# Kernel optimization log

Hardware: AMD Instinct MI355X
Metric: run time of the kernel (lower is better)

## Reference

```python
import jax, jax.numpy as jnp
import numpy as np

DIM = 768
DEPTH = 12
HEADS = 12
PATCH = 16
IMG = 256
CIN = 3
HID = 4 * DIM
EPS = 1e-6


def rmsnorm(x, w):
    return x * jax.lax.rsqrt(jnp.mean(x * x, axis=-1, keepdims=True) + EPS) * w


def ste(x, xq):
    # straight-through estimator: forward uses quantized value
    return x + jax.lax.stop_gradient(xq - x)


def bit_linear(x, w):
    # BitNet b1.58: ternary weights (per-tensor absmean scale) + int8 per-token activations
    w_scale = jnp.mean(jnp.abs(w)) + 1e-5
    w_q = jnp.clip(jnp.round(w / w_scale), -1.0, 1.0) * w_scale
    w_dq = ste(w, w_q)
    x_scale = 127.0 / jnp.clip(jnp.max(jnp.abs(x), axis=-1, keepdims=True), 1e-5)
    x_q = jnp.clip(jnp.round(x * x_scale), -128.0, 127.0) / x_scale
    x_dq = ste(x, x_q)
    return x_dq @ w_dq.T


def time_embedding(t, t_w1, t_b1, t_w2, t_b2):
    half = DIM // 2
    freqs = jnp.exp(-jnp.log(10000.0) * jnp.arange(half, dtype=jnp.float32) / (half - 1))
    args = t[:, None] * freqs[None, :]
    emb = jnp.concatenate([jnp.sin(args), jnp.cos(args)], axis=-1)
    h = jax.nn.gelu(emb @ t_w1.T + t_b1)
    return h @ t_w2.T + t_b2


def dit_block(x, t_emb, n1, qkv_w, proj_w, n2, fc1_w, fc2_w, ada_w, ada_b):
    B, N, C = x.shape
    hd = C // HEADS
    mod = jax.nn.silu(t_emb) @ ada_w.T + ada_b  # [B, 4*C]
    shift1, scale1, shift2, scale2 = jnp.split(mod, 4, axis=-1)
    # attention branch
    h = rmsnorm(x, n1)
    h = h * (1.0 + scale1[:, None, :]) + shift1[:, None, :]
    qkv = bit_linear(h, qkv_w).reshape(B, N, 3, HEADS, hd)
    q, k, v = qkv[:, :, 0], qkv[:, :, 1], qkv[:, :, 2]  # [B, N, H, hd]
    attn = jnp.einsum('bnhd,bmhd->bhnm', q, k) * (hd ** -0.5)
    attn = jax.nn.softmax(attn, axis=-1)
    o = jnp.einsum('bhnm,bmhd->bnhd', attn, v).reshape(B, N, C)
    x = x + bit_linear(o, proj_w)
    # mlp branch
    h = rmsnorm(x, n2)
    h = h * (1.0 + scale2[:, None, :]) + shift2[:, None, :]
    h = jax.nn.gelu(bit_linear(h, fc1_w))
    x = x + bit_linear(h, fc2_w)
    return x


def setup_inputs() -> dict:
    key = jax.random.key(0)
    ks = jax.random.split(key, 20)
    s = 0.02
    patch_dim = CIN * PATCH * PATCH
    inp = {
        'x': jax.random.normal(ks[0], (16, CIN, IMG, IMG), jnp.float32),
        't': jax.random.uniform(ks[1], (16,), jnp.float32) * 1000.0,
        'patch_w': jax.random.normal(ks[2], (DIM, patch_dim), jnp.float32) * s,
        'patch_b': jnp.zeros((DIM,), jnp.float32),
        'pos_embed': jax.random.normal(ks[3], (1, (IMG // PATCH) ** 2, DIM), jnp.float32) * s,
        't_w1': jax.random.normal(ks[4], (DIM, DIM), jnp.float32) * s,
        't_b1': jnp.zeros((DIM,), jnp.float32),
        't_w2': jax.random.normal(ks[5], (DIM, DIM), jnp.float32) * s,
        't_b2': jnp.zeros((DIM,), jnp.float32),
        'blk_norm1': jnp.ones((DEPTH, DIM), jnp.float32),
        'blk_qkv': jax.random.normal(ks[6], (DEPTH, 3 * DIM, DIM), jnp.float32) * s,
        'blk_proj': jax.random.normal(ks[7], (DEPTH, DIM, DIM), jnp.float32) * s,
        'blk_norm2': jnp.ones((DEPTH, DIM), jnp.float32),
        'blk_fc1': jax.random.normal(ks[8], (DEPTH, HID, DIM), jnp.float32) * s,
        'blk_fc2': jax.random.normal(ks[9], (DEPTH, DIM, HID), jnp.float32) * s,
        'blk_ada_w': jax.random.normal(ks[10], (DEPTH, 4 * DIM, DIM), jnp.float32) * s,
        'blk_ada_b': jnp.zeros((DEPTH, 4 * DIM), jnp.float32),
        'norm_w': jnp.ones((DIM,), jnp.float32),
        'head_w': jax.random.normal(ks[11], (patch_dim, DIM), jnp.float32) * s,
        'head_b': jnp.zeros((patch_dim,), jnp.float32),
    }
    return inp


def reference(x, t, patch_w, patch_b, pos_embed, t_w1, t_b1, t_w2, t_b2,
              blk_norm1, blk_qkv, blk_proj, blk_norm2, blk_fc1, blk_fc2,
              blk_ada_w, blk_ada_b, norm_w, head_w, head_b):
    B, C, H, W = x.shape
    p = PATCH
    h = H // p
    w = W // p
    # patchify: [B, C, H, W] -> [B, N, C*p*p]
    xp = x.reshape(B, C, h, p, w, p).transpose(0, 2, 4, 1, 3, 5).reshape(B, h * w, C * p * p)
    z = xp @ patch_w.T + patch_b + pos_embed
    t_emb = time_embedding(t, t_w1, t_b1, t_w2, t_b2)
    for i in range(DEPTH):
        z = dit_block(z, t_emb, blk_norm1[i], blk_qkv[i], blk_proj[i],
                      blk_norm2[i], blk_fc1[i], blk_fc2[i], blk_ada_w[i], blk_ada_b[i])
    z = rmsnorm(z, norm_w)
    z = z @ head_w.T + head_b  # [B, N, C*p*p]
    # unpatchify
    out = z.reshape(B, h, w, C, p, p).transpose(0, 3, 1, 4, 2, 5).reshape(B, C, H, W)
    return out
```

## Files before the change

kernel.cpp:

```cpp
#include <hip/hip_runtime.h>
#include <cstdint>

#define NTOK   4096
#define CDIM   768
#define NHID   3072
#define NHEADS 12

typedef int i32x4 __attribute__((ext_vector_type(4)));

__device__ __forceinline__ float4 ld4(const float* p){ return *(const float4*)(p); }

__device__ __forceinline__ float gelu_f(float x){
  float x3 = x*x*x;
  return 0.5f*x*(1.0f + tanhf(0.7978845608028654f*(x + 0.044715f*x3)));
}

template<bool ISMAX>
__device__ __forceinline__ float block_reduce(float v, float* red){
  #pragma unroll
  for (int o = 32; o > 0; o >>= 1){
    float w = __shfl_down(v, o);
    v = ISMAX ? fmaxf(v, w) : (v + w);
  }
  int wid = threadIdx.x >> 6;
  if ((threadIdx.x & 63) == 0) red[wid] = v;
  __syncthreads();
  float r = ISMAX ? fmaxf(fmaxf(red[0], red[1]), fmaxf(red[2], red[3]))
                  : (red[0] + red[1] + red[2] + red[3]);
  __syncthreads();
  return r;
}

__device__ __forceinline__ const float* layer_base(int type, int blk,
    const float* wqkv, const float* wproj, const float* wfc1, const float* wfc2,
    long* n_out, long* qoff_out)
{
  switch (type){
    case 0:  *n_out = 2304L*768; *qoff_out = 0;       return wqkv  + (long)blk*2304*768;
    case 1:  *n_out = 768L*768;  *qoff_out = 1769472; return wproj + (long)blk*768*768;
    case 2:  *n_out = 3072L*768; *qoff_out = 2359296; return wfc1  + (long)blk*3072*768;
    default: *n_out = 768L*3072; *qoff_out = 4718592; return wfc2  + (long)blk*768*3072;
  }
}

__global__ __launch_bounds__(256) void k_wabs_reduce(
  const float* __restrict__ wqkv, const float* __restrict__ wproj,
  const float* __restrict__ wfc1, const float* __restrict__ wfc2,
  float* __restrict__ acc)
{
  __shared__ float red[4];
  int layer = blockIdx.y, blk = layer >> 2, type = layer & 3;
  long n, qoff;
  const float* base = layer_base(type, blk, wqkv, wproj, wfc1, wfc2, &n, &qoff);
  long i0 = ((long)blockIdx.x*256 + threadIdx.x)*8;
  float s = 0.f;
  if (i0 < n){
    float4 a = ld4(base+i0), b = ld4(base+i0+4);
    s = fabsf(a.x)+fabsf(a.y)+fabsf(a.z)+fabsf(a.w)
      + fabsf(b.x)+fabsf(b.y)+fabsf(b.z)+fabsf(b.w);
  }
  s = block_reduce<false>(s, red);
  if (threadIdx.x == 0 && s != 0.f) atomicAdd(&acc[layer], s);
}

__global__ void k_wscale(const float* __restrict__ acc, float* __restrict__ wsc){
  int l = threadIdx.x;
  if (l < 48){
    const float cnt[4] = {2304.f*768.f, 768.f*768.f, 3072.f*768.f, 768.f*3072.f};
    wsc[l] = acc[l]/cnt[l & 3] + 1e-5f;
  }
}

__global__ __launch_bounds__(256) void k_wquant_write(
  const float* __restrict__ wqkv, const float* __restrict__ wproj,
  const float* __restrict__ wfc1, const float* __restrict__ wfc2,
  const float* __restrict__ wsc, signed char* __restrict__ wq)
{
  int layer = blockIdx.y, blk = layer >> 2, type = layer & 3;
  long n, qoff;
  const float* base = layer_base(type, blk, wqkv, wproj, wfc1, wfc2, &n, &qoff);
  long i0 = ((long)blockIdx.x*256 + threadIdx.x)*8;
  if (i0 >= n) return;
  signed char* dst = wq + (long)blk*7077888 + qoff;
  float ws = wsc[layer];
  float4 a = ld4(base+i0), b = ld4(base+i0+4);
  float v[8] = {a.x,a.y,a.z,a.w,b.x,b.y,b.z,b.w};
  long pk;
  char* pc = (char*)&pk;
  #pragma unroll
  for (int e = 0; e < 8; e++){
    float r = rintf(v[e] / ws);
    r = fminf(1.f, fmaxf(-1.f, r));
    pc[e] = (char)(int)r;
  }
  *(long*)(dst + i0) = pk;
}

__global__ __launch_bounds__(256) void k_patchify(const float* __restrict__ x, float* __restrict__ xp){
  int idx = blockIdx.x*256 + threadIdx.x;
  int col = idx % 768, row = idx / 768;
  int bb = row >> 8, pr = row & 255, ph = pr >> 4, pw = pr & 15;
  int c = col >> 8, rem = col & 255, ii = rem >> 4, jj = rem & 15;
  xp[idx] = x[(((long)(bb*3 + c) << 8) + (ph<<4) + ii)*256 + (pw<<4) + jj];
}

__global__ __launch_bounds__(256) void k_unpatchify(const float* __restrict__ H, float* __restrict__ out){
  int idx = blockIdx.x*256 + threadIdx.x;
  int xc = idx & 255;
  int y  = (idx >> 8) & 255;
  int bc = idx >> 16;
  int bb = bc / 3, c = bc % 3;
  int row = (bb << 8) + ((y >> 4) << 4) + (xc >> 4);
  int col = (c << 8) + ((y & 15) << 4) + (xc & 15);
  out[idx] = H[(long)row*768 + col];
}

__global__ __launch_bounds__(256) void k_time_full(
  const float* __restrict__ tt, const float* __restrict__ w1, const float* __restrict__ b1,
  const float* __restrict__ w2, const float* __restrict__ b2,
  float* __restrict__ temb, float* __restrict__ silu)
{
  __shared__ float emb[768];
  __shared__ float h1[768];
  int b = blockIdx.x, tid = threadIdx.x;
  float tv = tt[b];
  for (int i = tid; i < 768; i += 256){
    int idx = (i < 384) ? i : (i - 384);
    float fr = expf(-9.210340371976184f * (float)idx / 383.f);
    float a = tv * fr;
    emb[i] = (i < 384) ? sinf(a) : cosf(a);
  }
  __syncthreads();
  for (int o = tid; o < 768; o += 256){
    const float* wr = w1 + (long)o*768;
    float s = b1[o];
    for (int d = 0; d < 768; d += 4){
      float4 w4 = ld4(wr+d);
      s += w4.x*emb[d] + w4.y*emb[d+1] + w4.z*emb[d+2] + w4.w*emb[d+3];
    }
    h1[o] = gelu_f(s);
  }
  __syncthreads();
  for (int o = tid; o < 768; o += 256){
    const float* wr = w2 + (long)o*768;
    float s = b2[o];
    for (int d = 0; d < 768; d += 4){
      float4 w4 = ld4(wr+d);
      s += w4.x*h1[d] + w4.y*h1[d+1] + w4.z*h1[d+2] + w4.w*h1[d+3];
    }
    temb[b*768 + o] = s;
    silu[b*768 + o] = s / (1.f + expf(-s));
  }
}

__global__ __launch_bounds__(256) void k_mod_all(
  const float* __restrict__ silu, const float* __restrict__ wada, const float* __restrict__ bada,
  float* __restrict__ mod)
{
  __shared__ float ss[12288];
  int l = blockIdx.y, ch = blockIdx.x, tid = threadIdx.x;
  for (int i = tid; i < 12288; i += 256) ss[i] = silu[i];
  __syncthreads();
  int r = (ch << 8) + tid;
  const float* wr = wada + ((long)l*3072 + r)*768;
  float accv[16];
  #pragma unroll
  for (int b2 = 0; b2 < 16; b2++) accv[b2] = 0.f;
  for (int d = 0; d < 768; d += 4){
    float4 w4 = ld4(wr+d);
    #pragma unroll
    for (int b2 = 0; b2 < 16; b2++){
      float4 s4 = *(const float4*)&ss[b2*768 + d];
      accv[b2] += w4.x*s4.x + w4.y*s4.y + w4.z*s4.z + w4.w*s4.w;
    }
  }
  float bb = bada[(long)l*3072 + r];
  #pragma unroll
  for (int b2 = 0; b2 < 16; b2++)
    mod[((long)l*16 + b2)*3072 + r] = accv[b2] + bb;
}

__global__ __launch_bounds__(256) void k_rmsnorm_mod_quant(
  const float* __restrict__ Z, const float* __restrict__ nw,
  const float* __restrict__ mod, int mod_off,
  signed char* __restrict__ XQ, float* __restrict__ XS)
{
  __shared__ float red[4];
  int row = blockIdx.x, tid = threadIdx.x;
  int b = row >> 8;
  const float* zr = Z + (long)row*768;
  const float* mo = mod + (long)b*3072 + mod_off;
  float v[3]; float ss = 0.f;
  #pragma unroll
  for (int k = 0; k < 3; k++){ v[k] = zr[tid + k*256]; ss += v[k]*v[k]; }
  ss = block_reduce<false>(ss, red);
  float rms = rsqrtf(ss*(1.f/768.f) + 1e-6f);
  float h[3]; float amax = 0.f;
  #pragma unroll
  for (int k = 0; k < 3; k++){
    int c = tid + k*256;
    h[k] = v[k]*rms*nw[c]*(1.f + mo[768 + c]) + mo[c];
    amax = fmaxf(amax, fabsf(h[k]));
  }
  amax = block_reduce<true>(amax, red);
  float xs = 127.f / fmaxf(amax, 1e-5f);
  #pragma unroll
  for (int k = 0; k < 3; k++){
    int q = (int)rintf(h[k]*xs);
    q = min(127, max(-128, q));
    XQ[(long)row*768 + tid + k*256] = (signed char)q;
  }
  if (tid == 0) XS[row] = xs;
}

template<int W>
__global__ __launch_bounds__(256) void k_quant_rows(
  const float* __restrict__ X, signed char* __restrict__ XQ, float* __restrict__ XS)
{
  __shared__ float red[4];
  int row = blockIdx.x, tid = threadIdx.x;
  const float* xr = X + (long)row*W;
  constexpr int E = W/256;
  float v[E]; float amax = 0.f;
  #pragma unroll
  for (int k = 0; k < E; k++){ v[k] = xr[tid + k*256]; amax = fmaxf(amax, fabsf(v[k])); }
  amax = block_reduce<true>(amax, red);
  float xs = 127.f / fmaxf(amax, 1e-5f);
  #pragma unroll
  for (int k = 0; k < E; k++){
    int q = (int)rintf(v[k]*xs);
    q = min(127, max(-128, q));
    XQ[(long)row*W + tid + k*256] = (signed char)q;
  }
  if (tid == 0) XS[row] = xs;
}

__global__ __launch_bounds__(256) void k_rmsnorm_final(
  const float* __restrict__ Z, const float* __restrict__ nw, float* __restrict__ Y)
{
  __shared__ float red[4];
  int row = blockIdx.x, tid = threadIdx.x;
  const float* zr = Z + (long)row*768;
  float v[3]; float ss = 0.f;
  #pragma unroll
  for (int k = 0; k < 3; k++){ v[k] = zr[tid + k*256]; ss += v[k]*v[k]; }
  ss = block_reduce<false>(ss, red);
  float rms = rsqrtf(ss*(1.f/768.f) + 1e-6f);
  #pragma unroll
  for (int k = 0; k < 3; k++){
    int c = tid + k*256;
    Y[(long)row*768 + c] = v[k]*rms*nw[c];
  }
}

#define GLDS16(g, l) __builtin_amdgcn_global_load_lds( \
    (const __attribute__((address_space(1))) void*)(g), \
    (__attribute__((address_space(3))) void*)(l), 16, 0, 0)

template<int EPI>
__global__ __launch_bounds__(256, 2) void k_gemm_i8(
  const signed char* __restrict__ A, const signed char* __restrict__ Bw,
  const float* __restrict__ xs, const float* __restrict__ wsc_p,
  float* __restrict__ C, int N, int K)
{
  __shared__ signed char As[8192];
  __shared__ signed char Bs[8192];
  const int tid = threadIdx.x;
  const int w = tid >> 6, l = tid & 63;
  const int m0 = blockIdx.y << 7, n0 = blockIdx.x << 7;
  const float wsc = wsc_p[0];
  i32x4 acc[4][4] = {};
  const int srow = (w << 5) + (l >> 2);
  const int scol = (l & 3) << 4;
  const signed char* Ag0 = A  + (long)(m0 + srow)*K + scol;
  const signed char* Bg0 = Bw + (long)(n0 + srow)*K + scol;
  const long row16 = 16L*K;
  signed char* lA0 = As + (w << 11);
  signed char* lA1 = lA0 + 1024;
  signed char* lB0 = Bs + (w << 11);
  signed char* lB1 = lB0 + 1024;
  const int fr = l & 15;
  const int fc = (l >> 4) << 4;
  const int wm = (w >> 1) << 6, wn = (w & 1) << 6;

  for (int kt = 0; kt < K; kt += 64){
    __syncthreads();
    GLDS16(Ag0 + kt, lA0);
    GLDS16(Ag0 + row16 + kt, lA1);
    GLDS16(Bg0 + kt, lB0);
    GLDS16(Bg0 + row16 + kt, lB1);
    __syncthreads();
    i32x4 af[4], bf[4];
    #pragma unroll
    for (int mi = 0; mi < 4; mi++) af[mi] = *(const i32x4*)(As + ((wm + (mi<<4) + fr) << 6) + fc);
    #pragma unroll
    for (int ni = 0; ni < 4; ni++) bf[ni] = *(const i32x4*)(Bs + ((wn + (ni<<4) + fr) << 6) + fc);
    #pragma unroll
    for (int mi = 0; mi < 4; mi++)
      #pragma unroll
      for (int ni = 0; ni < 4; ni++)
        acc[mi][ni] = __builtin_amdgcn_mfma_i32_16x16x64_i8(af[mi], bf[ni], acc[mi][ni], 0, 0, 0);
  }

  const int cr0 = m0 + wm + ((l >> 4) << 2);
  const int cc0 = n0 + wn + fr;
  #pragma unroll
  for (int mi = 0; mi < 4; mi++){
    float rf[4];
    #pragma unroll
    for (int j = 0; j < 4; j++) rf[j] = wsc / xs[cr0 + (mi<<4) + j];
    #pragma unroll
    for (int ni = 0; ni < 4; ni++){
      int col = cc0 + (ni<<4);
      #pragma unroll
      for (int j = 0; j < 4; j++){
        long row = cr0 + (mi<<4) + j;
        float vv = (float)acc[mi][ni][j] * rf[j];
        if (EPI == 0)      C[row*N + col] = vv;
        else if (EPI == 1) C[row*N + col] += vv;
        else               C[row*N + col] = gelu_f(vv);
      }
    }
  }
}

template<int EPI>
__global__ __launch_bounds__(256) void k_sgemm(
  const float* __restrict__ A, const float* __restrict__ W,
  const float* __restrict__ bias, const float* __restrict__ pos,
  float* __restrict__ C, int N, int K)
{
  __shared__ float As[16][132];
  __shared__ float Bs[16][132];
  const int tid = threadIdx.x;
  const int tx = tid & 15, ty = tid >> 4;
  const int m0 = blockIdx.y << 7, n0 = blockIdx.x << 7;
  const int srow = tid >> 2, scol = (tid & 3) << 2;
  float acc[8][8] = {};
  const float* Ag0 = A + (long)(m0 + srow)*K + scol;
  const float* Ag1 = A + (long)(m0 + 64 + srow)*K + scol;
  const float* Bg0 = W + (long)(n0 + srow)*K + scol;
  const float* Bg1 = W + (long)(n0 + 64 + srow)*K + scol;

  for (int kt = 0; kt < K; kt += 16){
    float4 a0 = ld4(Ag0 + kt), a1 = ld4(Ag1 + kt);
    float4 b0 = ld4(Bg0 + kt), b1 = ld4(Bg1 + kt);
    __syncthreads();
    As[scol+0][srow] = a0.x; As[scol+1][srow] = a0.y; As[scol+2][srow] = a0.z; As[scol+3][srow] = a0.w;
    As[scol+0][64+srow] = a1.x; As[scol+1][64+srow] = a1.y; As[scol+2][64+srow] = a1.z; As[scol+3][64+srow] = a1.w;
    Bs[scol+0][srow] = b0.x; Bs[scol+1][srow] = b0.y; Bs[scol+2][srow] = b0.z; Bs[scol+3][srow] = b0.w;
    Bs[scol+0][64+srow] = b1.x; Bs[scol+1][64+srow] = b1.y; Bs[scol+2][64+srow] = b1.z; Bs[scol+3][64+srow] = b1.w;
    __syncthreads();
    #pragma unroll
    for (int k = 0; k < 16; k++){
      float a[8], b[8];
      *(float4*)&a[0] = *(const float4*)&As[k][ty*8];
      *(float4*)&a[4] = *(const float4*)&As[k][ty*8 + 4];
      *(float4*)&b[0] = *(const float4*)&Bs[k][tx*4];
      *(float4*)&b[4] = *(const float4*)&Bs[k][64 + tx*4];
      #pragma unroll
      for (int i = 0; i < 8; i++)
        #pragma unroll
        for (int j = 0; j < 8; j++)
          acc[i][j] = fmaf(a[i], b[j], acc[i][j]);
    }
  }

  #pragma unroll
  for (int i = 0; i < 8; i++){
    int row = m0 + ty*8 + i;
    float* cp = C + (long)row*N;
    #pragma unroll
    for (int half = 0; half < 2; half++){
      int c0 = n0 + half*64 + tx*4;
      float o[4];
      #pragma unroll
      for (int j = 0; j < 4; j++){
        o[j] = acc[i][half*4 + j] + bias[c0 + j];
        if (EPI == 0) o[j] += pos[(long)(row & 255)*768 + c0 + j];
      }
      *(float4*)(cp + c0) = *(float4*)o;
    }
  }
}

__global__ __launch_bounds__(256, 2) void k_attn(const float* __restrict__ QKV, float* __restrict__ O)
{
  __shared__ float Qs[64][68];
  __shared__ float Ks[64][68];
  __shared__ float Vs[64][68];
  __shared__ float Ps[64][68];
  const int tid = threadIdx.x;
  const int qt = blockIdx.x & 3;
  const int h  = (blockIdx.x >> 2) % NHEADS;
  const int b  = blockIdx.x / (4*NHEADS);
  const int r  = tid >> 2, c4 = tid & 3;
  const int wswz = (r >> 4) << 2;
  const int rswz = c4 << 2;

  {
    const float* qsrc = QKV + (long)((b << 8) + (qt << 6) + r)*2304 + (h << 6) + (c4 << 4);
    #pragma unroll
    for (int q = 0; q < 4; q++){
      float4 t = ld4(qsrc + q*4);
      t.x *= 0.125f; t.y *= 0.125f; t.z *= 0.125f; t.w *= 0.125f;
      *(float4*)&Qs[r][(c4 << 4) + q*4] = t;
    }
  }

  float4 oa[4];
  #pragma unroll
  for (int q = 0; q < 4; q++) oa[q] = make_float4(0.f, 0.f, 0.f, 0.f);
  float m_run = -3.0e38f, l_run = 0.f;
  const float* kbase = QKV + (long)((b << 8) + r)*2304 + 768 + (h << 6) + (c4 << 4);

  for (int kt = 0; kt < 4; ++kt){
    __syncthreads();
    const float* ksrc = kbase + (long)(kt << 6)*2304;
    #pragma unroll
    for (int q = 0; q < 4; q++){
      float4 kk = ld4(ksrc + q*4);
      *(float4*)&Ks[r][(((c4 << 4) + q*4) ^ wswz)] = kk;
      float4 vv = ld4(ksrc + 768 + q*4);
      *(float4*)&Vs[r][(c4 << 4) + q*4] = vv;
    }
    __syncthreads();

    float s[16];
    #pragma unroll
    for (int jj = 0; jj < 16; jj++) s[jj] = 0.f;
    const int jbase = c4 << 4;
    for (int d = 0; d < 64; d += 4){
      float4 q4 = *(const float4*)&Qs[r][d];
      #pragma unroll
      for (int jj = 0; jj < 16; jj++){
        float4 k4 = *(const float4*)&Ks[jbase + jj][d ^ rswz];
        s[jj] = fmaf(q4.x, k4.x, fmaf(q4.y, k4.y, fmaf(q4.z, k4.z, fmaf(q4.w, k4.w, s[jj]))));
      }
    }

    float mt = s[0];
    #pragma unroll
    for (int jj = 1; jj < 16; jj++) mt = fmaxf(mt, s[jj]);
    mt = fmaxf(mt, __shfl_xor(mt, 1));
    mt = fmaxf(mt, __shfl_xor(mt, 2));
    float m_new = fmaxf(m_run, mt);
    float alpha = __expf(m_run - m_new);
    float psum = 0.f;
    #pragma unroll
    for (int jj = 0; jj < 16; jj++){
      float p = __expf(s[jj] - m_new);
      psum += p;
      Ps[r][jbase + jj] = p;
    }
    psum += __shfl_xor(psum, 1);
    psum += __shfl_xor(psum, 2);
    l_run = l_run*alpha + psum;
    m_run = m_new;
    #pragma unroll
    for (int q = 0; q < 4; q++){
      oa[q].x *= alpha; oa[q].y *= alpha; oa[q].z *= alpha; oa[q].w *= alpha;
    }
    __syncthreads();
    #pragma unroll 4
    for (int kv = 0; kv < 64; ++kv){
      float p = Ps[r][kv];
      #pragma unroll
      for (int q = 0; q < 4; q++){
        float4 v4 = *(const float4*)&Vs[kv][(c4 << 4) + q*4];
        oa[q].x = fmaf(p, v4.x, oa[q].x);
        oa[q].y = fmaf(p, v4.y, oa[q].y);
        oa[q].z = fmaf(p, v4.z, oa[q].z);
        oa[q].w = fmaf(p, v4.w, oa[q].w);
      }
    }
  }

  float inv = 1.f / l_run;
  float* dst = O + (long)((b << 8) + (qt << 6) + r)*768 + (h << 6) + (c4 << 4);
  #pragma unroll
  for (int q = 0; q < 4; q++){
    float4 t = oa[q];
    t.x *= inv; t.y *= inv; t.z *= inv; t.w *= inv;
    *(float4*)(dst + q*4) = t;
  }
}

constexpr size_t WQ_OFF  = 0;
constexpr size_t WQ_SZ   = 84934656ULL;
constexpr size_t ACC_OFF = WQ_OFF + WQ_SZ;
constexpr size_t WS_OFF  = ACC_OFF + 256;
constexpr size_t Z_OFF   = WS_OFF + 256;
constexpr size_t XP_OFF  = Z_OFF + 12582912ULL;
constexpr size_t BIG_OFF = XP_OFF + 12582912ULL;
constexpr size_t AO_OFF  = BIG_OFF + 50331648ULL;
constexpr size_t XQ_OFF  = AO_OFF + 12582912ULL;
constexpr size_t XS_OFF  = XQ_OFF + 12582912ULL;
constexpr size_t TE_OFF  = XS_OFF + 16384;
constexpr size_t SI_OFF  = TE_OFF + 49152;
constexpr size_t MOD_OFF = SI_OFF + 49152;

extern "C" void kernel_launch(void* const* d_in, const int* in_sizes, int n_in,
                              void* d_out, int out_size, void* d_ws, size_t ws_size,
                              hipStream_t stream)
{
  (void)in_sizes; (void)n_in; (void)out_size; (void)ws_size;
  const float* x       = (const float*)d_in[0];
  const float* t       = (const float*)d_in[1];
  const float* patch_w = (const float*)d_in[2];
  const float* patch_b = (const float*)d_in[3];
  const float* pos     = (const float*)d_in[4];
  const float* t_w1    = (const float*)d_in[5];
  const float* t_b1    = (const float*)d_in[6];
  const float* t_w2    = (const float*)d_in[7];
  const float* t_b2    = (const float*)d_in[8];
  const float* n1      = (const float*)d_in[9];
  const float* wqkv    = (const float*)d_in[10];
  const float* wproj   = (const float*)d_in[11];
  const float* n2      = (const float*)d_in[12];
  const float* wfc1    = (const float*)d_in[13];
  const float* wfc2    = (const float*)d_in[14];
  const float* wada    = (const float*)d_in[15];
  const float* bada    = (const float*)d_in[16];
  const float* norm_w  = (const float*)d_in[17];
  const float* head_w  = (const float*)d_in[18];
  const float* head_b  = (const float*)d_in[19];
  float* out = (float*)d_out;

  char* ws = (char*)d_ws;
  signed char* WQ  = (signed char*)(ws + WQ_OFF);
  float* ACC = (float*)(ws + ACC_OFF);
  float* WSC = (float*)(ws + WS_OFF);
  float* Z   = (float*)(ws + Z_OFF);
  float* XP  = (float*)(ws + XP_OFF);
  float* BIG = (float*)(ws + BIG_OFF);
  float* AO  = (float*)(ws + AO_OFF);
  signed char* XQ = (signed char*)(ws + XQ_OFF);
  float* XS  = (float*)(ws + XS_OFF);
  float* TE  = (float*)(ws + TE_OFF);
  float* SI  = (float*)(ws + SI_OFF);
  float* MODP = (float*)(ws + MOD_OFF);

  hipMemsetAsync(ACC, 0, 48*sizeof(float), stream);
  dim3 gq(1152, 48);
  k_wabs_reduce<<<gq, 256, 0, stream>>>(wqkv, wproj, wfc1, wfc2, ACC);
  k_wscale<<<1, 64, 0, stream>>>(ACC, WSC);
  k_wquant_write<<<gq, 256, 0, stream>>>(wqkv, wproj, wfc1, wfc2, WSC, WQ);

  k_patchify<<<12288, 256, 0, stream>>>(x, XP);
  k_sgemm<0><<<dim3(6, 32), 256, 0, stream>>>(XP, patch_w, patch_b, pos, Z, 768, 768);

  k_time_full<<<16, 256, 0, stream>>>(t, t_w1, t_b1, t_w2, t_b2, TE, SI);
  k_mod_all<<<dim3(12, 12), 256, 0, stream>>>(SI, wada, bada, MODP);

  for (int i = 0; i < 12; i++){
    const float* n1i  = n1 + i*768;
    const float* n2i  = n2 + i*768;
    const float* modi = MODP + (size_t)i*16*3072;
    const signed char* wq_qkv  = WQ + (size_t)i*7077888 + 0;
    const signed char* wq_proj = WQ + (size_t)i*7077888 + 1769472;
    const signed char* wq_fc1  = WQ + (size_t)i*7077888 + 2359296;
    const signed char* wq_fc2  = WQ + (size_t)i*7077888 + 4718592;
    const float* ws_i = WSC + i*4;

    k_rmsnorm_mod_quant<<<4096, 256, 0, stream>>>(Z, n1i, modi, 0, XQ, XS);
    k_gemm_i8<0><<<dim3(18, 32), 256, 0, stream>>>(XQ, wq_qkv, XS, ws_i + 0, BIG, 2304, 768);
    k_attn<<<768, 256, 0, stream>>>(BIG, AO);
    k_quant_rows<768><<<4096, 256, 0, stream>>>(AO, XQ, XS);
    k_gemm_i8<1><<<dim3(6, 32), 256, 0, stream>>>(XQ, wq_proj, XS, ws_i + 1, Z, 768, 768);
    k_rmsnorm_mod_quant<<<4096, 256, 0, stream>>>(Z, n2i, modi, 1536, XQ, XS);
    k_gemm_i8<2><<<dim3(24, 32), 256, 0, stream>>>(XQ, wq_fc1, XS, ws_i + 2, BIG, 3072, 768);
    k_quant_rows<3072><<<4096, 256, 0, stream>>>(BIG, XQ, XS);
    k_gemm_i8<1><<<dim3(6, 32), 256, 0, stream>>>(XQ, wq_fc2, XS, ws_i + 3, Z, 768, 3072);
  }

  k_rmsnorm_final<<<4096, 256, 0, stream>>>(Z, norm_w, XP);
  k_sgemm<1><<<dim3(6, 32), 256, 0, stream>>>(XP, head_w, head_b, nullptr, BIG, 768, 768);
  k_unpatchify<<<12288, 256, 0, stream>>>(BIG, out);
}
```

Baseline: 3.971 ms.

## Split-K the residual int8 GEMMs and grid-stride the weight quantization kernels

The proj and fc2 int8 GEMMs, which have only 192 output tiles, now split K across two blocks along grid z and accumulate into the residual with atomicAdd. This is meant to raise occupancy on a 256-CU device. The weight abs-sum and quantization kernels become grid-stride loops with far fewer blocks and wider 16-byte stores, which cuts atomic traffic and launch overhead. An unused time-embedding buffer write is also removed. Atomic float adds make the summation order nondeterministic and add contention on the output.

```diff
diff --git a/kernel.cpp b/kernel.cpp
--- a/kernel.cpp
+++ b/kernel.cpp
@@ -52,15 +52,15 @@
   int layer = blockIdx.y, blk = layer >> 2, type = layer & 3;
   long n, qoff;
   const float* base = layer_base(type, blk, wqkv, wproj, wfc1, wfc2, &n, &qoff);
-  long i0 = ((long)blockIdx.x*256 + threadIdx.x)*8;
   float s = 0.f;
-  if (i0 < n){
+  const long stride = 72L*256*8;
+  for (long i0 = ((long)blockIdx.x*256 + threadIdx.x)*8; i0 < n; i0 += stride){
     float4 a = ld4(base+i0), b = ld4(base+i0+4);
-    s = fabsf(a.x)+fabsf(a.y)+fabsf(a.z)+fabsf(a.w)
-      + fabsf(b.x)+fabsf(b.y)+fabsf(b.z)+fabsf(b.w);
+    s += fabsf(a.x)+fabsf(a.y)+fabsf(a.z)+fabsf(a.w)
+       + fabsf(b.x)+fabsf(b.y)+fabsf(b.z)+fabsf(b.w);
   }
   s = block_reduce<false>(s, red);
-  if (threadIdx.x == 0 && s != 0.f) atomicAdd(&acc[layer], s);
+  if (threadIdx.x == 0) atomicAdd(&acc[layer], s);
 }
 
 __global__ void k_wscale(const float* __restrict__ acc, float* __restrict__ wsc){
@@ -79,21 +79,25 @@
   int layer = blockIdx.y, blk = layer >> 2, type = layer & 3;
   long n, qoff;
   const float* base = layer_base(type, blk, wqkv, wproj, wfc1, wfc2, &n, &qoff);
-  long i0 = ((long)blockIdx.x*256 + threadIdx.x)*8;
-  if (i0 >= n) return;
   signed char* dst = wq + (long)blk*7077888 + qoff;
   float ws = wsc[layer];
-  float4 a = ld4(base+i0), b = ld4(base+i0+4);
-  float v[8] = {a.x,a.y,a.z,a.w,b.x,b.y,b.z,b.w};
-  long pk;
-  char* pc = (char*)&pk;
-  #pragma unroll
-  for (int e = 0; e < 8; e++){
-    float r = rintf(v[e] / ws);
-    r = fminf(1.f, fmaxf(-1.f, r));
-    pc[e] = (char)(int)r;
-  }
-  *(long*)(dst + i0) = pk;
+  const long stride = 36L*256*16;
+  for (long i0 = ((long)blockIdx.x*256 + threadIdx.x)*16; i0 < n; i0 += stride){
+    float v[16];
+    *(float4*)&v[0]  = ld4(base+i0);
+    *(float4*)&v[4]  = ld4(base+i0+4);
+    *(float4*)&v[8]  = ld4(base+i0+8);
+    *(float4*)&v[12] = ld4(base+i0+12);
+    i32x4 pk;
+    char* pc = (char*)&pk;
+    #pragma unroll
+    for (int e = 0; e < 16; e++){
+      float r = rintf(v[e] / ws);
+      r = fminf(1.f, fmaxf(-1.f, r));
+      pc[e] = (char)(int)r;
+    }
+    *(i32x4*)(dst + i0) = pk;
+  }
 }
 
 __global__ __launch_bounds__(256) void k_patchify(const float* __restrict__ x, float* __restrict__ xp){
@@ -118,7 +122,7 @@
 __global__ __launch_bounds__(256) void k_time_full(
   const float* __restrict__ tt, const float* __restrict__ w1, const float* __restrict__ b1,
   const float* __restrict__ w2, const float* __restrict__ b2,
-  float* __restrict__ temb, float* __restrict__ silu)
+  float* __restrict__ silu)
 {
   __shared__ float emb[768];
   __shared__ float h1[768];
@@ -148,8 +152,8 @@
       float4 w4 = ld4(wr+d);
       s += w4.x*h1[d] + w4.y*h1[d+1] + w4.z*h1[d+2] + w4.w*h1[d+3];
     }
-    temb[b*768 + o] = s;
-    silu[b*768 + o] = s / (1.f + expf(-s));
+    float te = s;
+    silu[b*768 + o] = te / (1.f + expf(-te));
   }
 }
 
@@ -257,7 +261,7 @@
     (const __attribute__((address_space(1))) void*)(g), \
     (__attribute__((address_space(3))) void*)(l), 16, 0, 0)
 
-template<int EPI>
+template<int EPI, int NSPLIT>
 __global__ __launch_bounds__(256, 2) void k_gemm_i8(
   const signed char* __restrict__ A, const signed char* __restrict__ Bw,
   const float* __restrict__ xs, const float* __restrict__ wsc_p,
@@ -283,7 +287,11 @@
   const int fc = (l >> 4) << 4;
   const int wm = (w >> 1) << 6, wn = (w & 1) << 6;
 
-  for (int kt = 0; kt < K; kt += 64){
+  const int Ksp = K / NSPLIT;
+  const int k_begin = (NSPLIT > 1) ? (int)blockIdx.z * Ksp : 0;
+  const int k_end = k_begin + Ksp;
+
+  for (int kt = k_begin; kt < k_end; kt += 64){
     __syncthreads();
     GLDS16(Ag0 + kt, lA0);
     GLDS16(Ag0 + row16 + kt, lA1);
@@ -317,7 +325,10 @@
         long row = cr0 + (mi<<4) + j;
         float vv = (float)acc[mi][ni][j] * rf[j];
         if (EPI == 0)      C[row*N + col] = vv;
-        else if (EPI == 1) C[row*N + col] += vv;
+        else if (EPI == 1){
+          if (NSPLIT > 1)  atomicAdd(&C[row*N + col], vv);
+          else             C[row*N + col] += vv;
+        }
         else               C[row*N + col] = gelu_f(vv);
       }
     }
@@ -496,8 +507,7 @@
 constexpr size_t AO_OFF  = BIG_OFF + 50331648ULL;
 constexpr size_t XQ_OFF  = AO_OFF + 12582912ULL;
 constexpr size_t XS_OFF  = XQ_OFF + 12582912ULL;
-constexpr size_t TE_OFF  = XS_OFF + 16384;
-constexpr size_t SI_OFF  = TE_OFF + 49152;
+constexpr size_t SI_OFF  = XS_OFF + 16384;
 constexpr size_t MOD_OFF = SI_OFF + 49152;
 
 extern "C" void kernel_launch(void* const* d_in, const int* in_sizes, int n_in,
@@ -537,20 +547,18 @@
   float* AO  = (float*)(ws + AO_OFF);
   signed char* XQ = (signed char*)(ws + XQ_OFF);
   float* XS  = (float*)(ws + XS_OFF);
-  float* TE  = (float*)(ws + TE_OFF);
   float* SI  = (float*)(ws + SI_OFF);
   float* MODP = (float*)(ws + MOD_OFF);
 
   hipMemsetAsync(ACC, 0, 48*sizeof(float), stream);
-  dim3 gq(1152, 48);
-  k_wabs_reduce<<<gq, 256, 0, stream>>>(wqkv, wproj, wfc1, wfc2, ACC);
+  k_wabs_reduce<<<dim3(72, 48), 256, 0, stream>>>(wqkv, wproj, wfc1, wfc2, ACC);
   k_wscale<<<1, 64, 0, stream>>>(ACC, WSC);
-  k_wquant_write<<<gq, 256, 0, stream>>>(wqkv, wproj, wfc1, wfc2, WSC, WQ);
+  k_wquant_write<<<dim3(36, 48), 256, 0, stream>>>(wqkv, wproj, wfc1, wfc2, WSC, WQ);
 
   k_patchify<<<12288, 256, 0, stream>>>(x, XP);
   k_sgemm<0><<<dim3(6, 32), 256, 0, stream>>>(XP, patch_w, patch_b, pos, Z, 768, 768);
 
-  k_time_full<<<16, 256, 0, stream>>>(t, t_w1, t_b1, t_w2, t_b2, TE, SI);
+  k_time_full<<<16, 256, 0, stream>>>(t, t_w1, t_b1, t_w2, t_b2, SI);
   k_mod_all<<<dim3(12, 12), 256, 0, stream>>>(SI, wada, bada, MODP);
 
   for (int i = 0; i < 12; i++){
@@ -564,14 +572,14 @@
     const float* ws_i = WSC + i*4;
 
     k_rmsnorm_mod_quant<<<4096, 256, 0, stream>>>(Z, n1i, modi, 0, XQ, XS);
-    k_gemm_i8<0><<<dim3(18, 32), 256, 0, stream>>>(XQ, wq_qkv, XS, ws_i + 0, BIG, 2304, 768);
+    k_gemm_i8<0,1><<<dim3(18, 32), 256, 0, stream>>>(XQ, wq_qkv, XS, ws_i + 0, BIG, 2304, 768);
     k_attn<<<768, 256, 0, stream>>>(BIG, AO);
     k_quant_rows<768><<<4096, 256, 0, stream>>>(AO, XQ, XS);
-    k_gemm_i8<1><<<dim3(6, 32), 256, 0, stream>>>(XQ, wq_proj, XS, ws_i + 1, Z, 768, 768);
+    k_gemm_i8<1,2><<<dim3(6, 32, 2), 256, 0, stream>>>(XQ, wq_proj, XS, ws_i + 1, Z, 768, 768);
     k_rmsnorm_mod_quant<<<4096, 256, 0, stream>>>(Z, n2i, modi, 1536, XQ, XS);
-    k_gemm_i8<2><<<dim3(24, 32), 256, 0, stream>>>(XQ, wq_fc1, XS, ws_i + 2, BIG, 3072, 768);
+    k_gemm_i8<2,1><<<dim3(24, 32), 256, 0, stream>>>(XQ, wq_fc1, XS, ws_i + 2, BIG, 3072, 768);
     k_quant_rows<3072><<<4096, 256, 0, stream>>>(BIG, XQ, XS);
-    k_gemm_i8<1><<<dim3(6, 32), 256, 0, stream>>>(XQ, wq_fc2, XS, ws_i + 3, Z, 768, 3072);
+    k_gemm_i8<1,2><<<dim3(6, 32, 2), 256, 0, stream>>>(XQ, wq_fc2, XS, ws_i + 3, Z, 768, 3072);
   }
 
   k_rmsnorm_final<<<4096, 256, 0, stream>>>(Z, norm_w, XP);
```

Result: faster. 3.612 ms (-9.0%).
